# Kernel tuning notes

Measured on AMD Instinct MI355X. Metric: run time of the kernel, lower is better.

Reference implementation:

```python
import jax, jax.numpy as jnp
import numpy as np

DEC = 1024
MEM = 1024


def setup_inputs() -> dict:
    key = jax.random.key(0)
    k1, k2, k3, k4, k5 = jax.random.split(key, 5)
    decoder_state = jax.random.normal(k1, (64, DEC), dtype=jnp.float32)
    memory_bank = jax.random.normal(k2, (64, 2048, MEM), dtype=jnp.float32)
    src_mask = jnp.ones((64, 2048), dtype=jnp.int32)
    # learned params (torch Linear: y = x @ W.T); store as (in, out) for einsum
    s = 1.0 / np.sqrt(DEC)
    W_v = jax.random.uniform(k3, (DEC,), jnp.float32, -s, s)            # v: decoder_size -> 1
    W_dec = jax.random.uniform(k4, (DEC, DEC), jnp.float32, -s, s)       # decode_project
    sm = 1.0 / np.sqrt(MEM)
    W_mem = jax.random.uniform(k5, (MEM, DEC), jnp.float32, -sm, sm)     # memory_project
    return {"decoder_state": decoder_state, "memory_bank": memory_bank,
            "src_mask": src_mask, "W_v": W_v, "W_dec": W_dec, "W_mem": W_mem}


def reference(decoder_state, memory_bank, src_mask, W_v, W_dec, W_mem):
    # encoder_feature: [B,S,D]; dec_feature: [B,D]
    enc_feat = jnp.einsum('bsm,md->bsd', memory_bank, W_mem)
    dec_feat = jnp.einsum('bm,md->bd', decoder_state, W_dec)
    e = jnp.tanh(enc_feat + dec_feat[:, None, :])      # [B,S,D]
    scores = jnp.einsum('bsd,d->bs', e, W_v)           # [B,S]
    scores = jnp.where(src_mask == 0, -jnp.inf, scores)
    attn_dist = jax.nn.softmax(scores, axis=-1)        # [B,S]
    context = jnp.einsum('bs,bsm->bm', attn_dist, memory_bank)  # [B,M]
    return (context, attn_dist)
```

## Files before the change

### kernel.cpp

```cpp
#include <hip/hip_runtime.h>

typedef __bf16 bf16;
typedef __bf16 bf16x8 __attribute__((ext_vector_type(8)));
typedef float f32x4 __attribute__((ext_vector_type(4)));

constexpr int kB = 64;
constexpr int kS = 2048;
constexpr int kD = 1024;
constexpr int kM = 1024;
constexpr int kRows = kB * kS;

__device__ __forceinline__ void async_copy16(const void* gsrc, void* ldst) {
    __builtin_amdgcn_global_load_lds(
        (const __attribute__((address_space(1))) void*)gsrc,
        (__attribute__((address_space(3))) void*)ldst, 16, 0, 0);
}

__device__ __forceinline__ float fast_tanh(float x) {
    float e = __expf(2.0f * x);
    return 1.0f - 2.0f * __builtin_amdgcn_rcpf(e + 1.0f);
}

__global__ __launch_bounds__(256) void wmem_transpose_kernel(
    const float* __restrict__ Wm, bf16* __restrict__ WT) {
    int idx = blockIdx.x * 256 + threadIdx.x;
    int d = idx >> 10, m = idx & 1023;
    WT[idx] = (bf16)Wm[m * 1024 + d];
}

__global__ __launch_bounds__(256) void dec_project_kernel(
    const float* __restrict__ dec, const float* __restrict__ Wd,
    float* __restrict__ decf) {
    const int b = blockIdx.x;
    const int d = blockIdx.y * 256 + threadIdx.x;
    const float* drow = dec + b * kD;
    float acc = 0.f;
    #pragma unroll 8
    for (int m = 0; m < kM; ++m)
        acc += drow[m] * Wd[(size_t)m * kD + d];
    decf[b * kD + d] = acc;
}

constexpr int BM = 128, BN = 128, BK = 32, APAD = 40;

__global__ __launch_bounds__(256, 2) void attn_scores_kernel(
    const float* __restrict__ MBank,
    const bf16*  __restrict__ WT,
    const float* __restrict__ decf,
    const float* __restrict__ Wv,
    float* __restrict__ spart)
{
    __shared__ bf16 Atile[BM * APAD];
    __shared__ bf16 Btile[BN * BK];
    __shared__ float sred[BM * 2];

    const int tid  = threadIdx.x;
    const int wave = tid >> 6;
    const int lane = tid & 63;
    const int ln   = lane & 15;
    const int quad = lane >> 4;

    const int colTile = blockIdx.x;
    const int rowTile = blockIdx.y;
    const int R0 = rowTile * BM;
    const int C0 = colTile * BN;
    const int batch = rowTile >> 4;

    const int wr = (wave >> 1) * 64;
    const int wc = (wave & 1) * 64;

    const int arow  = tid >> 1;
    const int akseg = (tid & 1) * 16;
    const float* aptr = MBank + (size_t)(R0 + arow) * kM + akseg;

    f32x4 acc[4][4];
    const f32x4 zero = {0.f, 0.f, 0.f, 0.f};
    #pragma unroll
    for (int i = 0; i < 4; ++i)
        #pragma unroll
        for (int j = 0; j < 4; ++j)
            acc[i][j] = zero;

    for (int k0 = 0; k0 < kM; k0 += BK) {
        __syncthreads();
        #pragma unroll
        for (int j = 0; j < 2; ++j) {
            const int chunk = wave * 2 + j;
            const int n = chunk * 16 + (lane >> 2);
            async_copy16(WT + (size_t)(C0 + n) * kM + k0 + (lane & 3) * 8,
                         Btile + chunk * 512);
        }
        {
            const float* ap = aptr + k0;
            f32x4 v0 = *(const f32x4*)(ap + 0);
            f32x4 v1 = *(const f32x4*)(ap + 4);
            f32x4 v2 = *(const f32x4*)(ap + 8);
            f32x4 v3 = *(const f32x4*)(ap + 12);
            bf16x8 w0, w1;
            w0[0]=(bf16)v0[0]; w0[1]=(bf16)v0[1]; w0[2]=(bf16)v0[2]; w0[3]=(bf16)v0[3];
            w0[4]=(bf16)v1[0]; w0[5]=(bf16)v1[1]; w0[6]=(bf16)v1[2]; w0[7]=(bf16)v1[3];
            w1[0]=(bf16)v2[0]; w1[1]=(bf16)v2[1]; w1[2]=(bf16)v2[2]; w1[3]=(bf16)v2[3];
            w1[4]=(bf16)v3[0]; w1[5]=(bf16)v3[1]; w1[6]=(bf16)v3[2]; w1[7]=(bf16)v3[3];
            *(bf16x8*)(Atile + arow * APAD + akseg)     = w0;
            *(bf16x8*)(Atile + arow * APAD + akseg + 8) = w1;
        }
        __syncthreads();

        bf16x8 af[4], bfr[4];
        #pragma unroll
        for (int i = 0; i < 4; ++i)
            af[i] = *(const bf16x8*)(Atile + (wr + i * 16 + ln) * APAD + quad * 8);
        #pragma unroll
        for (int j = 0; j < 4; ++j)
            bfr[j] = *(const bf16x8*)(Btile + (wc + j * 16 + ln) * BK + quad * 8);
        #pragma unroll
        for (int i = 0; i < 4; ++i)
            #pragma unroll
            for (int j = 0; j < 4; ++j)
                acc[i][j] = __builtin_amdgcn_mfma_f32_16x16x32_bf16(
                    af[i], bfr[j], acc[i][j], 0, 0, 0);
    }

    float wv[4], df[4];
    #pragma unroll
    for (int j = 0; j < 4; ++j) {
        const int d = C0 + wc + j * 16 + ln;
        wv[j] = Wv[d];
        df[j] = decf[batch * kD + d];
    }
    float rp[4][4];
    #pragma unroll
    for (int i = 0; i < 4; ++i) {
        #pragma unroll
        for (int r = 0; r < 4; ++r) {
            float p = 0.f;
            #pragma unroll
            for (int j = 0; j < 4; ++j) {
                float x = acc[i][j][r] + df[j];
                p += fast_tanh(x) * wv[j];
            }
            #pragma unroll
            for (int off = 1; off < 16; off <<= 1)
                p += __shfl_xor(p, off, 64);
            rp[i][r] = p;
        }
    }
    if (ln == 0) {
        #pragma unroll
        for (int i = 0; i < 4; ++i)
            #pragma unroll
            for (int r = 0; r < 4; ++r)
                sred[(wr + i * 16 + quad * 4 + r) * 2 + (wave & 1)] = rp[i][r];
    }
    __syncthreads();
    if (tid < BM)
        spart[(size_t)colTile * kRows + R0 + tid] = sred[tid * 2] + sred[tid * 2 + 1];
}

__global__ __launch_bounds__(256) void softmax_kernel(
    const float* __restrict__ spart, const int* __restrict__ mask,
    float* __restrict__ attn) {
    const int b = blockIdx.x;
    const int tid = threadIdx.x;
    __shared__ float sc[kS];
    __shared__ float redm[4], reds[4];

    float lmax = -INFINITY;
    for (int s = tid; s < kS; s += 256) {
        float v = 0.f;
        #pragma unroll
        for (int t = 0; t < 8; ++t) v += spart[(size_t)t * kRows + b * kS + s];
        if (mask[b * kS + s] == 0) v = -INFINITY;
        sc[s] = v;
        lmax = fmaxf(lmax, v);
    }
    #pragma unroll
    for (int off = 32; off; off >>= 1) lmax = fmaxf(lmax, __shfl_xor(lmax, off, 64));
    if ((tid & 63) == 0) redm[tid >> 6] = lmax;
    __syncthreads();
    const float bmax = fmaxf(fmaxf(redm[0], redm[1]), fmaxf(redm[2], redm[3]));

    float lsum = 0.f;
    for (int s = tid; s < kS; s += 256) {
        float e = __expf(sc[s] - bmax);
        sc[s] = e;
        lsum += e;
    }
    #pragma unroll
    for (int off = 32; off; off >>= 1) lsum += __shfl_xor(lsum, off, 64);
    if ((tid & 63) == 0) reds[tid >> 6] = lsum;
    __syncthreads();
    const float inv = 1.0f / (reds[0] + reds[1] + reds[2] + reds[3]);
    for (int s = tid; s < kS; s += 256) attn[b * kS + s] = sc[s] * inv;
}

__global__ __launch_bounds__(256) void ctx_partial_kernel(
    const float* __restrict__ MBank, const float* __restrict__ attn,
    float* __restrict__ cpart) {
    const int b  = blockIdx.x;
    const int sc = blockIdx.y;
    const int m4 = threadIdx.x * 4;
    const float* base = MBank + ((size_t)b * kS + sc * 128) * kM + m4;
    const float* ap = attn + b * kS + sc * 128;
    f32x4 acc = {0.f, 0.f, 0.f, 0.f};
    #pragma unroll 4
    for (int s = 0; s < 128; ++s) {
        const float a = ap[s];
        f32x4 v = *(const f32x4*)(base + (size_t)s * kM);
        acc[0] += a * v[0]; acc[1] += a * v[1];
        acc[2] += a * v[2]; acc[3] += a * v[3];
    }
    *(f32x4*)&cpart[((size_t)(b * 16 + sc)) * kM + m4] = acc;
}

__global__ __launch_bounds__(256) void ctx_reduce_kernel(
    const float* __restrict__ cpart, float* __restrict__ out) {
    const int idx = blockIdx.x * 256 + threadIdx.x;
    const int b = idx >> 10, m = idx & 1023;
    float v = 0.f;
    #pragma unroll
    for (int c = 0; c < 16; ++c) v += cpart[(size_t)((b * 16 + c) << 10) + m];
    out[idx] = v;
}

extern "C" void kernel_launch(void* const* d_in, const int* in_sizes, int n_in,
                              void* d_out, int out_size, void* d_ws, size_t ws_size,
                              hipStream_t stream) {
    const float* dec   = (const float*)d_in[0];
    const float* MBank = (const float*)d_in[1];
    const int*   mask  = (const int*)d_in[2];
    const float* Wv    = (const float*)d_in[3];
    const float* Wdec  = (const float*)d_in[4];
    const float* Wmem  = (const float*)d_in[5];

    float* out_ctx  = (float*)d_out;
    float* out_attn = (float*)d_out + kB * kD;

    char* ws = (char*)d_ws;
    bf16*  WT    = (bf16*)ws;
    float* decf  = (float*)(ws + (1 << 21));
    float* spart = (float*)(ws + (1 << 21) + (1 << 18));
    float* cpart = (float*)(ws + (1 << 21) + (1 << 18) + (1 << 22));

    wmem_transpose_kernel<<<4096, 256, 0, stream>>>(Wmem, WT);
    dec_project_kernel<<<dim3(64, 4), 256, 0, stream>>>(dec, Wdec, decf);
    attn_scores_kernel<<<dim3(8, 1024), 256, 0, stream>>>(MBank, WT, decf, Wv, spart);
    softmax_kernel<<<64, 256, 0, stream>>>(spart, mask, out_attn);
    ctx_partial_kernel<<<dim3(64, 16), 256, 0, stream>>>(MBank, out_attn, cpart);
    ctx_reduce_kernel<<<256, 256, 0, stream>>>(cpart, out_ctx);
}
```

Baseline: 1.279 ms.

## Hold full 64-row A slab in LDS and sweep all columns per block

The scores kernel is restructured so each block loads a 64-row slice of the memory bank once, converts it to bf16 into a 128KB XOR-swizzled LDS tile, and computes all 1024 output columns in two passes. B fragments are read straight from global memory with register double-buffering. The next slice's A is prefetched while MFMAs run. This removes the 8x re-read and re-conversion of the fp32 memory bank across column tiles and the partial-score buffer. The transpose and dec-projection kernels get tiled/split-K versions, and the ctx loop unroll is raised. Costs: occupancy drops to one block per CU because of the large LDS footprint and 64 accumulator vectors per thread, and every B fragment now comes from global/L2 instead of LDS.

After: 1.603 ms. 1.25x slower.

```diff
diff --git a/kernel.cpp b/kernel.cpp
--- a/kernel.cpp
+++ b/kernel.cpp
@@ -2,6 +2,7 @@
 
 typedef __bf16 bf16;
 typedef __bf16 bf16x8 __attribute__((ext_vector_type(8)));
+typedef __bf16 bf16x4 __attribute__((ext_vector_type(4)));
 typedef float f32x4 __attribute__((ext_vector_type(4)));
 
 constexpr int kB = 64;
@@ -10,12 +11,6 @@
 constexpr int kM = 1024;
 constexpr int kRows = kB * kS;
 
-__device__ __forceinline__ void async_copy16(const void* gsrc, void* ldst) {
-    __builtin_amdgcn_global_load_lds(
-        (const __attribute__((address_space(1))) void*)gsrc,
-        (__attribute__((address_space(3))) void*)ldst, 16, 0, 0);
-}
-
 __device__ __forceinline__ float fast_tanh(float x) {
     float e = __expf(2.0f * x);
     return 1.0f - 2.0f * __builtin_amdgcn_rcpf(e + 1.0f);
@@ -23,36 +18,54 @@
 
 __global__ __launch_bounds__(256) void wmem_transpose_kernel(
     const float* __restrict__ Wm, bf16* __restrict__ WT) {
-    int idx = blockIdx.x * 256 + threadIdx.x;
-    int d = idx >> 10, m = idx & 1023;
-    WT[idx] = (bf16)Wm[m * 1024 + d];
+    __shared__ float tile[64][65];
+    const int tc = blockIdx.x;
+    const int tr = blockIdx.y;
+    const int lw = threadIdx.x >> 6;
+    const int ll = threadIdx.x & 63;
+    #pragma unroll
+    for (int ii = 0; ii < 16; ++ii) {
+        const int lr = ii * 4 + lw;
+        tile[lr][ll] = Wm[(size_t)(tr * 64 + lr) * 1024 + tc * 64 + ll];
+    }
+    __syncthreads();
+    #pragma unroll
+    for (int ii = 0; ii < 16; ++ii) {
+        const int ld = ii * 4 + lw;
+        WT[(size_t)(tc * 64 + ld) * 1024 + tr * 64 + ll] = (bf16)tile[ll][ld];
+    }
 }
 
 __global__ __launch_bounds__(256) void dec_project_kernel(
     const float* __restrict__ dec, const float* __restrict__ Wd,
     float* __restrict__ decf) {
-    const int b = blockIdx.x;
-    const int d = blockIdx.y * 256 + threadIdx.x;
+    __shared__ float red[4][64];
+    const int b  = blockIdx.x;
+    const int dg = blockIdx.y;
+    const int d  = dg * 64 + (threadIdx.x & 63);
+    const int mq = threadIdx.x >> 6;
     const float* drow = dec + b * kD;
     float acc = 0.f;
     #pragma unroll 8
-    for (int m = 0; m < kM; ++m)
+    for (int m = mq * 256; m < (mq + 1) * 256; ++m)
         acc += drow[m] * Wd[(size_t)m * kD + d];
-    decf[b * kD + d] = acc;
-}
-
-constexpr int BM = 128, BN = 128, BK = 32, APAD = 40;
-
-__global__ __launch_bounds__(256, 2) void attn_scores_kernel(
+    red[mq][threadIdx.x & 63] = acc;
+    __syncthreads();
+    if (threadIdx.x < 64)
+        decf[b * kD + dg * 64 + threadIdx.x] =
+            red[0][threadIdx.x] + red[1][threadIdx.x] +
+            red[2][threadIdx.x] + red[3][threadIdx.x];
+}
+
+__global__ __launch_bounds__(256, 1) void attn_scores_kernel(
     const float* __restrict__ MBank,
     const bf16*  __restrict__ WT,
     const float* __restrict__ decf,
     const float* __restrict__ Wv,
-    float* __restrict__ spart)
+    float* __restrict__ scores)
 {
-    __shared__ bf16 Atile[BM * APAD];
-    __shared__ bf16 Btile[BN * BK];
-    __shared__ float sred[BM * 2];
+    __shared__ __align__(16) bf16 Atile[64 * 1024];
+    __shared__ float sred[64 * 4];
 
     const int tid  = threadIdx.x;
     const int wave = tid >> 6;
@@ -60,105 +73,121 @@
     const int ln   = lane & 15;
     const int quad = lane >> 4;
 
-    const int colTile = blockIdx.x;
-    const int rowTile = blockIdx.y;
-    const int R0 = rowTile * BM;
-    const int C0 = colTile * BN;
-    const int batch = rowTile >> 4;
-
-    const int wr = (wave >> 1) * 64;
-    const int wc = (wave & 1) * 64;
-
-    const int arow  = tid >> 1;
-    const int akseg = (tid & 1) * 16;
-    const float* aptr = MBank + (size_t)(R0 + arow) * kM + akseg;
-
-    f32x4 acc[4][4];
-    const f32x4 zero = {0.f, 0.f, 0.f, 0.f};
-    #pragma unroll
-    for (int i = 0; i < 4; ++i)
-        #pragma unroll
-        for (int j = 0; j < 4; ++j)
-            acc[i][j] = zero;
-
-    for (int k0 = 0; k0 < kM; k0 += BK) {
+    const int bid   = blockIdx.x;
+    const int R0    = bid * 64;
+    const int batch = bid >> 5;
+    const float* Ab = MBank + (size_t)R0 * kM;
+
+    f32x4 acc[2][4][8];
+    #pragma unroll
+    for (int c = 0; c < 2; ++c)
+        #pragma unroll
+        for (int i = 0; i < 4; ++i)
+            #pragma unroll
+            for (int j = 0; j < 8; ++j)
+                acc[c][i][j] = (f32x4){0.f, 0.f, 0.f, 0.f};
+
+    auto stageLoad = [&](int slice, int half, f32x4* v) {
+        #pragma unroll
+        for (int ii = 0; ii < 8; ++ii) {
+            const int row = half * 32 + ii * 4 + wave;
+            v[ii] = *(const f32x4*)(Ab + (size_t)row * kM + slice * 256 + lane * 4);
+        }
+    };
+    auto stageWrite = [&](int slice, int half, const f32x4* v) {
+        #pragma unroll
+        for (int ii = 0; ii < 8; ++ii) {
+            const int row = half * 32 + ii * 4 + wave;
+            const int u = slice * 32 + (lane >> 1);
+            bf16x4 w = {(bf16)v[ii][0], (bf16)v[ii][1],
+                        (bf16)v[ii][2], (bf16)v[ii][3]};
+            *(bf16x4*)(Atile + row * 1024 + ((u ^ (row & 7)) << 3) + (lane & 1) * 4) = w;
+        }
+    };
+    auto bload = [&](int ct, int k0, bf16x8* bfr) {
+        const bf16* bp = WT + (size_t)(ct * 512 + wave * 128 + ln) * 1024 + k0 + quad * 8;
+        #pragma unroll
+        for (int j = 0; j < 8; ++j)
+            bfr[j] = *(const bf16x8*)(bp + (size_t)j * 16 * 1024);
+    };
+    auto step = [&](int ct, int k0, const bf16x8* bfr) {
+        bf16x8 af[4];
+        const int ku = k0 >> 3;
+        #pragma unroll
+        for (int i = 0; i < 4; ++i) {
+            const int r = i * 16 + ln;
+            af[i] = *(const bf16x8*)(Atile + r * 1024 + (((ku + quad) ^ (ln & 7)) << 3));
+        }
+        #pragma unroll
+        for (int i = 0; i < 4; ++i)
+            #pragma unroll
+            for (int j = 0; j < 8; ++j)
+                acc[ct][i][j] = __builtin_amdgcn_mfma_f32_16x16x32_bf16(
+                    af[i], bfr[j], acc[ct][i][j], 0, 0, 0);
+    };
+
+    {
+        f32x4 v[8];
+        stageLoad(0, 0, v); stageWrite(0, 0, v);
+        stageLoad(0, 1, v); stageWrite(0, 1, v);
+    }
+
+    bf16x8 bb[2][8];
+    for (int kr = 0; kr < 4; ++kr) {
         __syncthreads();
-        #pragma unroll
-        for (int j = 0; j < 2; ++j) {
-            const int chunk = wave * 2 + j;
-            const int n = chunk * 16 + (lane >> 2);
-            async_copy16(WT + (size_t)(C0 + n) * kM + k0 + (lane & 3) * 8,
-                         Btile + chunk * 512);
-        }
-        {
-            const float* ap = aptr + k0;
-            f32x4 v0 = *(const f32x4*)(ap + 0);
-            f32x4 v1 = *(const f32x4*)(ap + 4);
-            f32x4 v2 = *(const f32x4*)(ap + 8);
-            f32x4 v3 = *(const f32x4*)(ap + 12);
-            bf16x8 w0, w1;
-            w0[0]=(bf16)v0[0]; w0[1]=(bf16)v0[1]; w0[2]=(bf16)v0[2]; w0[3]=(bf16)v0[3];
-            w0[4]=(bf16)v1[0]; w0[5]=(bf16)v1[1]; w0[6]=(bf16)v1[2]; w0[7]=(bf16)v1[3];
-            w1[0]=(bf16)v2[0]; w1[1]=(bf16)v2[1]; w1[2]=(bf16)v2[2]; w1[3]=(bf16)v2[3];
-            w1[4]=(bf16)v3[0]; w1[5]=(bf16)v3[1]; w1[6]=(bf16)v3[2]; w1[7]=(bf16)v3[3];
-            *(bf16x8*)(Atile + arow * APAD + akseg)     = w0;
-            *(bf16x8*)(Atile + arow * APAD + akseg + 8) = w1;
-        }
-        __syncthreads();
-
-        bf16x8 af[4], bfr[4];
-        #pragma unroll
-        for (int i = 0; i < 4; ++i)
-            af[i] = *(const bf16x8*)(Atile + (wr + i * 16 + ln) * APAD + quad * 8);
-        #pragma unroll
-        for (int j = 0; j < 4; ++j)
-            bfr[j] = *(const bf16x8*)(Btile + (wc + j * 16 + ln) * BK + quad * 8);
-        #pragma unroll
-        for (int i = 0; i < 4; ++i)
-            #pragma unroll
-            for (int j = 0; j < 4; ++j)
-                acc[i][j] = __builtin_amdgcn_mfma_f32_16x16x32_bf16(
-                    af[i], bfr[j], acc[i][j], 0, 0, 0);
-    }
-
-    float wv[4], df[4];
-    #pragma unroll
-    for (int j = 0; j < 4; ++j) {
-        const int d = C0 + wc + j * 16 + ln;
-        wv[j] = Wv[d];
-        df[j] = decf[batch * kD + d];
-    }
-    float rp[4][4];
+        const int kbase = kr * 256;
+        f32x4 v[8];
+        if (kr < 3) stageLoad(kr + 1, 0, v);
+        bload(0, kbase, bb[0]);
+        #pragma unroll
+        for (int idx = 0; idx < 16; ++idx) {
+            const int ct = idx >> 3;
+            const int k0 = kbase + (idx & 7) * 32;
+            if (idx == 8 && kr < 3) {
+                stageWrite(kr + 1, 0, v);
+                stageLoad(kr + 1, 1, v);
+            }
+            if (idx < 15)
+                bload((idx + 1) >> 3, kbase + ((idx + 1) & 7) * 32, bb[(idx + 1) & 1]);
+            step(ct, k0, bb[idx & 1]);
+        }
+        if (kr < 3) stageWrite(kr + 1, 1, v);
+    }
+
+    float wv[2][8], df[2][8];
+    #pragma unroll
+    for (int c = 0; c < 2; ++c)
+        #pragma unroll
+        for (int j = 0; j < 8; ++j) {
+            const int col = c * 512 + wave * 128 + j * 16 + ln;
+            wv[c][j] = Wv[col];
+            df[c][j] = decf[batch * kD + col];
+        }
     #pragma unroll
     for (int i = 0; i < 4; ++i) {
         #pragma unroll
         for (int r = 0; r < 4; ++r) {
             float p = 0.f;
             #pragma unroll
-            for (int j = 0; j < 4; ++j) {
-                float x = acc[i][j][r] + df[j];
-                p += fast_tanh(x) * wv[j];
-            }
+            for (int c = 0; c < 2; ++c)
+                #pragma unroll
+                for (int j = 0; j < 8; ++j)
+                    p += fast_tanh(acc[c][i][j][r] + df[c][j]) * wv[c][j];
             #pragma unroll
             for (int off = 1; off < 16; off <<= 1)
                 p += __shfl_xor(p, off, 64);
-            rp[i][r] = p;
-        }
-    }
-    if (ln == 0) {
-        #pragma unroll
-        for (int i = 0; i < 4; ++i)
-            #pragma unroll
-            for (int r = 0; r < 4; ++r)
-                sred[(wr + i * 16 + quad * 4 + r) * 2 + (wave & 1)] = rp[i][r];
-    }
-    __syncthreads();
-    if (tid < BM)
-        spart[(size_t)colTile * kRows + R0 + tid] = sred[tid * 2] + sred[tid * 2 + 1];
+            if (ln == 0)
+                sred[(i * 16 + quad * 4 + r) * 4 + wave] = p;
+        }
+    }
+    __syncthreads();
+    if (tid < 64)
+        scores[R0 + tid] = sred[tid * 4] + sred[tid * 4 + 1] +
+                           sred[tid * 4 + 2] + sred[tid * 4 + 3];
 }
 
 __global__ __launch_bounds__(256) void softmax_kernel(
-    const float* __restrict__ spart, const int* __restrict__ mask,
+    const float* __restrict__ scores, const int* __restrict__ mask,
     float* __restrict__ attn) {
     const int b = blockIdx.x;
     const int tid = threadIdx.x;
@@ -167,9 +196,7 @@
 
     float lmax = -INFINITY;
     for (int s = tid; s < kS; s += 256) {
-        float v = 0.f;
-        #pragma unroll
-        for (int t = 0; t < 8; ++t) v += spart[(size_t)t * kRows + b * kS + s];
+        float v = scores[b * kS + s];
         if (mask[b * kS + s] == 0) v = -INFINITY;
         sc[s] = v;
         lmax = fmaxf(lmax, v);
@@ -203,7 +230,7 @@
     const float* base = MBank + ((size_t)b * kS + sc * 128) * kM + m4;
     const float* ap = attn + b * kS + sc * 128;
     f32x4 acc = {0.f, 0.f, 0.f, 0.f};
-    #pragma unroll 4
+    #pragma unroll 8
     for (int s = 0; s < 128; ++s) {
         const float a = ap[s];
         f32x4 v = *(const f32x4*)(base + (size_t)s * kM);
@@ -237,15 +264,15 @@
     float* out_attn = (float*)d_out + kB * kD;
 
     char* ws = (char*)d_ws;
-    bf16*  WT    = (bf16*)ws;
-    float* decf  = (float*)(ws + (1 << 21));
-    float* spart = (float*)(ws + (1 << 21) + (1 << 18));
-    float* cpart = (float*)(ws + (1 << 21) + (1 << 18) + (1 << 22));
-
-    wmem_transpose_kernel<<<4096, 256, 0, stream>>>(Wmem, WT);
-    dec_project_kernel<<<dim3(64, 4), 256, 0, stream>>>(dec, Wdec, decf);
-    attn_scores_kernel<<<dim3(8, 1024), 256, 0, stream>>>(MBank, WT, decf, Wv, spart);
-    softmax_kernel<<<64, 256, 0, stream>>>(spart, mask, out_attn);
+    bf16*  WT     = (bf16*)ws;
+    float* decf   = (float*)(ws + (1 << 21));
+    float* scores = (float*)(ws + (1 << 21) + (1 << 18));
+    float* cpart  = (float*)(ws + (1 << 21) + (1 << 18) + (1 << 19));
+
+    wmem_transpose_kernel<<<dim3(16, 16), 256, 0, stream>>>(Wmem, WT);
+    dec_project_kernel<<<dim3(64, 16), 256, 0, stream>>>(dec, Wdec, decf);
+    attn_scores_kernel<<<2048, 256, 0, stream>>>(MBank, WT, decf, Wv, scores);
+    softmax_kernel<<<64, 256, 0, stream>>>(scores, mask, out_attn);
     ctx_partial_kernel<<<dim3(64, 16), 256, 0, stream>>>(MBank, out_attn, cpart);
     ctx_reduce_kernel<<<256, 256, 0, stream>>>(cpart, out_ctx);
 }
```
